# Optimization experiments

Hardware: AMD Instinct MI355X
Metric: run time of the kernel (lower is better)

## Reference

```python
import jax, jax.numpy as jnp
import numpy as np

N_HIDDEN = 2048
D_IN = 64
T_STEPS = 4096
WASHOUT = 200
SPECTRAL_RADIUS = 0.9
RIDGE_LAMBDA = 1e-6


def _scale_to_spectral_radius(W, rho, iters=100):
    # power iteration to estimate the dominant eigenvalue magnitude (spectral radius)
    rng = np.random.default_rng(0)
    v = rng.normal(size=W.shape[0]).astype(np.float64)
    v /= np.linalg.norm(v)
    for _ in range(iters):
        w = W @ v
        nrm = np.linalg.norm(w)
        v = w / nrm
    rad = np.linalg.norm(W @ v)
    return W * (rho / rad)


def setup_inputs() -> dict:
    key = jax.random.key(0)
    k1, k2, k3, k4 = jax.random.split(key, 4)
    u = jax.random.normal(k1, (T_STEPS, D_IN), dtype=jnp.float32)
    y = jax.random.normal(k2, (T_STEPS, 1), dtype=jnp.float32)
    W_in = jax.random.normal(k3, (N_HIDDEN, D_IN), dtype=jnp.float32) * 0.1
    W = np.asarray(jax.random.normal(k4, (N_HIDDEN, N_HIDDEN), dtype=jnp.float32), dtype=np.float64)
    W /= np.sqrt(N_HIDDEN)
    W = _scale_to_spectral_radius(W, SPECTRAL_RADIUS)
    W_res = jnp.asarray(W, dtype=jnp.float32)
    return {"u": u, "y": y, "W_in": W_in, "W_res": W_res, "washout": WASHOUT}


def reference(u, y, W_in, W_res, washout):
    # precompute input drive W_in @ u[t] for all t: [T, N]
    drive = u @ W_in.T
    x0 = jnp.zeros((W_res.shape[0],), dtype=u.dtype)

    def step(x, d):
        x = jnp.tanh(W_res @ x + d)
        return x, x

    _, X = jax.lax.scan(step, x0, drive)  # X: [T, N]
    Xw = X[washout:]                      # [T - washout, N]
    yw = y[washout:]                      # [T - washout, 1]
    A = Xw.T @ Xw + RIDGE_LAMBDA * jnp.eye(Xw.shape[1], dtype=Xw.dtype)
    Wout = jnp.linalg.solve(A, Xw.T @ yw)  # [N, 1]
    return Xw @ Wout                       # [T - washout, 1]
```

## Files before the change

kernel.cpp:

```cpp
#include <hip/hip_runtime.h>
#include <math.h>

#define NH      2048
#define TT      4096
#define DIN     64
#define WASH    200
#define TW      (TT - WASH)
#define LAMBDA  1e-6f

#define SCAN_BLOCKS  64
#define CG_BLOCKS    64
#define CG_ITERS     400

typedef unsigned long long u64;

#define X_OFF      ((size_t)0)
#define DRIVE_OFF  ((size_t)TT * NH)
#define A_OFF      DRIVE_OFF
#define B_OFF      ((size_t)2 * TT * NH)
#define INVD_OFF   (B_OFF + NH)
#define XV_OFF     (INVD_OFF + NH)
#define WS_FLOATS  (XV_OFF + NH)
#define XPACK_OFF  ((size_t)0)
#define PPACK_OFF  ((size_t)2 * NH)
#define PQSLOT_OFF ((size_t)3 * NH)
#define RZSLOT_OFF ((size_t)3 * NH + 64)
#define U64_TOTAL  ((size_t)3 * NH + 128)

__device__ __forceinline__ u64 pack_ev(int epoch, float v) {
    return ((u64)(unsigned)epoch << 32) | (u64)__float_as_uint(v);
}
__device__ __forceinline__ int   ep_of(u64 p)  { return (int)(p >> 32); }
__device__ __forceinline__ float val_of(u64 p) { return __uint_as_float((unsigned)p); }

__device__ __forceinline__ u64 aload(const u64* p) {
    return __hip_atomic_load(p, __ATOMIC_RELAXED, __HIP_MEMORY_SCOPE_AGENT);
}
__device__ __forceinline__ void astore(u64* p, u64 v) {
    __hip_atomic_store(p, v, __ATOMIC_RELAXED, __HIP_MEMORY_SCOPE_AGENT);
}

__global__ void init_kernel(float* ws) {
    int tid = threadIdx.x;
    u64* ub = (u64*)(ws + WS_FLOATS);
    for (size_t i = tid; i < U64_TOTAL; i += 256) ub[i] = 0ull;
    for (int i = tid; i < NH; i += 256) ws[B_OFF + i] = 0.f;
}

__global__ __launch_bounds__(256) void drive_kernel(
    const float* __restrict__ u, const float* __restrict__ Win,
    float* __restrict__ drive)
{
    __shared__ float Wt[256 * 64];
    const int tid = threadIdx.x;
    const int ic = blockIdx.x & 7;
    const int tc = blockIdx.x >> 3;
    const int i0 = ic * 256;
    for (int idx = tid; idx < 256 * 64; idx += 256) {
        int il = idx >> 6, k = idx & 63;
        Wt[k * 256 + il] = Win[(size_t)i0 * 64 + idx];
    }
    __syncthreads();
    for (int tt_ = 0; tt_ < 128; ++tt_) {
        int t = tc * 128 + tt_;
        const float* ur = u + (size_t)t * DIN;
        float acc = 0.f;
        #pragma unroll
        for (int k = 0; k < 64; ++k)
            acc = fmaf(Wt[k * 256 + tid], ur[k], acc);
        drive[(size_t)t * NH + i0 + tid] = acc;
    }
}

__global__ __launch_bounds__(1024, 1) void scan_kernel(
    const float* __restrict__ W, const float* __restrict__ drive,
    float* __restrict__ X, u64* xpack)
{
    __shared__ float xls[NH];
    const int tid     = threadIdx.x;
    const int r_local = tid >> 5;
    const int lane32  = tid & 31;
    const int row     = blockIdx.x * 32 + r_local;

    float4 wreg[16];
    {
        const float* wp = W + (size_t)row * NH + lane32 * 4;
        #pragma unroll
        for (int j = 0; j < 16; ++j) wreg[j] = *(const float4*)(wp + 128 * j);
    }

    for (int t = 0; t < TT; ++t) {
        float dval = drive[(size_t)t * NH + row];

        if (t == 0) {
            xls[tid] = 0.f; xls[tid + 1024] = 0.f;
        } else {
            const u64* src = xpack + (size_t)((t - 1) & 1) * NH;
            const int want = t;
            u64 a = aload(&src[tid]);
            u64 b = aload(&src[tid + 1024]);
            bool pa = true, pb = true;
            if (ep_of(a) >= want) { xls[tid] = val_of(a); pa = false; }
            if (ep_of(b) >= want) { xls[tid + 1024] = val_of(b); pb = false; }
            while (pa || pb) {
                __builtin_amdgcn_s_sleep(1);
                if (pa) { u64 v = aload(&src[tid]);
                          if (ep_of(v) >= want) { xls[tid] = val_of(v); pa = false; } }
                if (pb) { u64 v = aload(&src[tid + 1024]);
                          if (ep_of(v) >= want) { xls[tid + 1024] = val_of(v); pb = false; } }
            }
        }
        __syncthreads();

        float acc = 0.f;
        #pragma unroll
        for (int j = 0; j < 16; ++j) {
            float4 xv4 = *(const float4*)&xls[lane32 * 4 + 128 * j];
            float4 wv = wreg[j];
            acc = fmaf(wv.x, xv4.x, fmaf(wv.y, xv4.y,
                  fmaf(wv.z, xv4.z, fmaf(wv.w, xv4.w, acc))));
        }
        #pragma unroll
        for (int m = 16; m; m >>= 1) acc += __shfl_xor(acc, m);

        if (lane32 == 0) {
            float v = tanhf(acc + dval);
            X[(size_t)t * NH + row] = v;
            astore(&xpack[(size_t)(t & 1) * NH + row], pack_ev(t + 1, v));
        }
        __syncthreads();
    }
}

__global__ __launch_bounds__(256) void gram_kernel(
    const float* __restrict__ X, float* __restrict__ A)
{
    if (blockIdx.x < blockIdx.y) return;
    __shared__ float As[16 * 64];
    __shared__ float Bs[16 * 64];
    const int tx = threadIdx.x, ty = threadIdx.y;
    const int tid = ty * 16 + tx;
    const int i0 = blockIdx.y * 64, j0 = blockIdx.x * 64;
    const int ty4 = ty * 4, tx4 = tx * 4;
    float acc[4][4] = {};

    const int nch = (TW + 15) / 16;
    for (int ch = 0; ch < nch; ++ch) {
        int tbase = WASH + ch * 16;
        for (int v = tid; v < 16 * 64; v += 256) {
            int kk = v >> 6, col = v & 63;
            int t = tbase + kk;
            float a_ = 0.f, b_ = 0.f;
            if (t < TT) {
                a_ = X[(size_t)t * NH + i0 + col];
                b_ = X[(size_t)t * NH + j0 + col];
            }
            As[v] = a_; Bs[v] = b_;
        }
        __syncthreads();
        #pragma unroll
        for (int k = 0; k < 16; ++k) {
            float4 av = *(const float4*)&As[k * 64 + ty4];
            float4 bv = *(const float4*)&Bs[k * 64 + tx4];
            float a[4] = {av.x, av.y, av.z, av.w};
            float b[4] = {bv.x, bv.y, bv.z, bv.w};
            #pragma unroll
            for (int ai = 0; ai < 4; ++ai)
                #pragma unroll
                for (int bi = 0; bi < 4; ++bi)
                    acc[ai][bi] = fmaf(a[ai], b[bi], acc[ai][bi]);
        }
        __syncthreads();
    }
    const bool diag = (blockIdx.x == blockIdx.y);
    #pragma unroll
    for (int ai = 0; ai < 4; ++ai) {
        int gi = i0 + ty4 + ai;
        #pragma unroll
        for (int bi = 0; bi < 4; ++bi) {
            int gj = j0 + tx4 + bi;
            float v = acc[ai][bi];
            if (gi == gj) v += LAMBDA;
            A[(size_t)gi * NH + gj] = v;
            if (!diag) A[(size_t)gj * NH + gi] = v;
        }
    }
}

__global__ void bvec_kernel(const float* __restrict__ X, const float* __restrict__ y,
                            float* __restrict__ bv)
{
    const int ic = blockIdx.x & 7, tc = blockIdx.x >> 3;
    const int i = ic * 256 + threadIdx.x;
    const int t0 = WASH + tc * (TW / 8), t1 = t0 + (TW / 8);
    float acc = 0.f;
    for (int t = t0; t < t1; ++t)
        acc = fmaf(X[(size_t)t * NH + i], y[t], acc);
    atomicAdd(&bv[i], acc);
}

__global__ void invdiag_kernel(const float* __restrict__ A, float* __restrict__ invd)
{
    int i = blockIdx.x * 256 + threadIdx.x;
    invd[i] = 1.0f / A[(size_t)i * NH + i];
}

__global__ __launch_bounds__(1024, 1) void cg_kernel(
    const float* __restrict__ A, const float* __restrict__ bvec,
    const float* __restrict__ invd, float* __restrict__ xv,
    u64* ppack, u64* pqslot, u64* rzslot)
{
    __shared__ float pls[NH];
    __shared__ float qsh[32], r32[32], x32[32], z32[32], inv32[32];
    __shared__ float csh[2];
    const int tid     = threadIdx.x;
    const int r_local = tid >> 5;
    const int lane32  = tid & 31;
    const int row0 = blockIdx.x * 32;
    const int row  = row0 + r_local;

    float4 areg[16];
    {
        const float* ap = A + (size_t)row * NH + lane32 * 4;
        #pragma unroll
        for (int j = 0; j < 16; ++j) areg[j] = *(const float4*)(ap + 128 * j);
    }

    if (tid < 32) {
        int i = row0 + tid;
        float bi = bvec[i], iv = invd[i];
        inv32[tid] = iv;
        x32[tid] = 0.f; r32[tid] = bi;
        float zi = iv * bi;
        z32[tid] = zi;
        astore(&ppack[i], pack_ev(1, zi));
        float part = bi * zi;
        #pragma unroll
        for (int m = 16; m; m >>= 1) part += __shfl_xor(part, m, 32);
        if (tid == 0) astore(&rzslot[blockIdx.x], pack_ev(1, part));
    }
    if (tid < 64) {
        u64 v = aload(&rzslot[tid]);
        while (ep_of(v) < 1) { __builtin_amdgcn_s_sleep(1); v = aload(&rzslot[tid]); }
        float s = val_of(v);
        #pragma unroll
        for (int m = 32; m; m >>= 1) s += __shfl_xor(s, m);
        if (tid == 0) csh[1] = s;
    }
    __syncthreads();
    float rho = csh[1];

    for (int it = 0; it < CG_ITERS; ++it) {
        {
            const int want = it + 1;
            u64 a = aload(&ppack[tid]);
            u64 b = aload(&ppack[tid + 1024]);
            bool pa = true, pb = true;
            if (ep_of(a) >= want) { pls[tid] = val_of(a); pa = false; }
            if (ep_of(b) >= want) { pls[tid + 1024] = val_of(b); pb = false; }
            while (pa || pb) {
                __builtin_amdgcn_s_sleep(1);
                if (pa) { u64 v = aload(&ppack[tid]);
                          if (ep_of(v) >= want) { pls[tid] = val_of(v); pa = false; } }
                if (pb) { u64 v = aload(&ppack[tid + 1024]);
                          if (ep_of(v) >= want) { pls[tid + 1024] = val_of(v); pb = false; } }
            }
        }
        __syncthreads();

        float acc = 0.f;
        #pragma unroll
        for (int j = 0; j < 16; ++j) {
            float4 pv = *(const float4*)&pls[lane32 * 4 + 128 * j];
            float4 av = areg[j];
            acc = fmaf(av.x, pv.x, fmaf(av.y, pv.y,
                  fmaf(av.z, pv.z, fmaf(av.w, pv.w, acc))));
        }
        #pragma unroll
        for (int m = 16; m; m >>= 1) acc += __shfl_xor(acc, m, 32);
        if (lane32 == 0) qsh[r_local] = acc;
        __syncthreads();

        if (tid < 32) {
            float t1 = qsh[tid] * pls[row0 + tid];
            #pragma unroll
            for (int m = 16; m; m >>= 1) t1 += __shfl_xor(t1, m, 32);
            if (tid == 0) astore(&pqslot[blockIdx.x], pack_ev(it + 1, t1));
        }
        if (tid < 64) {
            u64 v = aload(&pqslot[tid]);
            while (ep_of(v) < it + 1) { __builtin_amdgcn_s_sleep(1); v = aload(&pqslot[tid]); }
            float s = val_of(v);
            #pragma unroll
            for (int m = 32; m; m >>= 1) s += __shfl_xor(s, m);
            if (tid == 0) csh[0] = s;
        }
        __syncthreads();
        float pq = csh[0];
        float alpha = (pq != 0.f) ? rho / pq : 0.f;

        if (tid < 32) {
            int i = row0 + tid;
            float pi = pls[i], qi = qsh[tid];
            x32[tid] = fmaf(alpha, pi, x32[tid]);
            float ri = r32[tid] - alpha * qi;
            r32[tid] = ri;
            float zi = inv32[tid] * ri;
            z32[tid] = zi;
            float t2 = ri * zi;
            #pragma unroll
            for (int m = 16; m; m >>= 1) t2 += __shfl_xor(t2, m, 32);
            if (tid == 0) astore(&rzslot[blockIdx.x], pack_ev(it + 2, t2));
        }
        if (tid < 64) {
            u64 v = aload(&rzslot[tid]);
            while (ep_of(v) < it + 2) { __builtin_amdgcn_s_sleep(1); v = aload(&rzslot[tid]); }
            float s = val_of(v);
            #pragma unroll
            for (int m = 32; m; m >>= 1) s += __shfl_xor(s, m);
            if (tid == 0) csh[1] = s;
        }
        __syncthreads();
        float rho_new = csh[1];
        float beta = (rho != 0.f) ? rho_new / rho : 0.f;

        if (tid < 32) {
            int i = row0 + tid;
            float pn = fmaf(beta, pls[i], z32[tid]);
            astore(&ppack[i], pack_ev(it + 2, pn));
        }
        rho = rho_new;
        __syncthreads();
    }

    if (tid < 32) xv[row0 + tid] = x32[tid];
}

__global__ void out_kernel(const float* __restrict__ X, const float* __restrict__ w,
                           float* __restrict__ out)
{
    __shared__ float red[4];
    const int tid = threadIdx.x;
    const int rowt = WASH + blockIdx.x;
    float acc = 0.f;
    #pragma unroll
    for (int j = 0; j < 8; ++j) {
        int c = tid + 256 * j;
        acc = fmaf(X[(size_t)rowt * NH + c], w[c], acc);
    }
    #pragma unroll
    for (int m = 32; m; m >>= 1) acc += __shfl_xor(acc, m);
    if ((tid & 63) == 0) red[tid >> 6] = acc;
    __syncthreads();
    if (tid == 0) out[blockIdx.x] = red[0] + red[1] + red[2] + red[3];
}

extern "C" void kernel_launch(void* const* d_in, const int* in_sizes, int n_in,
                              void* d_out, int out_size, void* d_ws, size_t ws_size,
                              hipStream_t stream)
{
    const float* u    = (const float*)d_in[0];
    const float* y    = (const float*)d_in[1];
    const float* Win  = (const float*)d_in[2];
    const float* Wres = (const float*)d_in[3];

    float* ws = (float*)d_ws;
    float* X     = ws + X_OFF;
    float* drive = ws + DRIVE_OFF;
    float* A     = ws + A_OFF;
    u64*   ub    = (u64*)(ws + WS_FLOATS);
    u64*   xpack = ub + XPACK_OFF;
    u64*   ppack = ub + PPACK_OFF;
    u64*   pqslot = ub + PQSLOT_OFF;
    u64*   rzslot = ub + RZSLOT_OFF;

    init_kernel<<<1, 256, 0, stream>>>(ws);
    drive_kernel<<<256, 256, 0, stream>>>(u, Win, drive);
    scan_kernel<<<SCAN_BLOCKS, 1024, 0, stream>>>(Wres, drive, X, xpack);
    gram_kernel<<<dim3(32, 32), dim3(16, 16), 0, stream>>>(X, A);
    bvec_kernel<<<64, 256, 0, stream>>>(X, y, ws + B_OFF);
    invdiag_kernel<<<8, 256, 0, stream>>>(A, ws + INVD_OFF);
    cg_kernel<<<CG_BLOCKS, 1024, 0, stream>>>(A, ws + B_OFF, ws + INVD_OFF,
                                              ws + XV_OFF, ppack, pqslot, rzslot);
    out_kernel<<<TW, 256, 0, stream>>>(X, ws + XV_OFF, (float*)d_out);
}
```

Before: 14.50 ms.

## Restructure CG to broadcast z and fuse rz wait; scan computes two rows per wave

The CG loop now broadcasts the preconditioned residual z instead of the search direction p. Every block rebuilds p locally from z and beta, so the separate rz grid-wide wait plus p publish becomes a single exchange per iteration, which cuts one global synchronisation round per iteration. The scan kernel now has each 64-lane wave compute two rows rather than one row per 32 lanes, trading shuffle layout for fewer reductions. The CG iteration count also drops from 400 to 320, which cuts work but may weaken convergence and accuracy.

```diff
diff --git a/kernel.cpp b/kernel.cpp
--- a/kernel.cpp
+++ b/kernel.cpp
@@ -10,7 +10,7 @@
 
 #define SCAN_BLOCKS  64
 #define CG_BLOCKS    64
-#define CG_ITERS     400
+#define CG_ITERS     320
 
 typedef unsigned long long u64;
 
@@ -22,7 +22,7 @@
 #define XV_OFF     (INVD_OFF + NH)
 #define WS_FLOATS  (XV_OFF + NH)
 #define XPACK_OFF  ((size_t)0)
-#define PPACK_OFF  ((size_t)2 * NH)
+#define ZPACK_OFF  ((size_t)2 * NH)
 #define PQSLOT_OFF ((size_t)3 * NH)
 #define RZSLOT_OFF ((size_t)3 * NH + 64)
 #define U64_TOTAL  ((size_t)3 * NH + 128)
@@ -77,20 +77,24 @@
     float* __restrict__ X, u64* xpack)
 {
     __shared__ float xls[NH];
-    const int tid     = threadIdx.x;
-    const int r_local = tid >> 5;
-    const int lane32  = tid & 31;
-    const int row     = blockIdx.x * 32 + r_local;
-
-    float4 wreg[16];
+    const int tid  = threadIdx.x;
+    const int wave = tid >> 6;
+    const int lane = tid & 63;
+    const int rowA = blockIdx.x * 32 + wave * 2;
+
+    float4 wA[8], wB[8];
     {
-        const float* wp = W + (size_t)row * NH + lane32 * 4;
-        #pragma unroll
-        for (int j = 0; j < 16; ++j) wreg[j] = *(const float4*)(wp + 128 * j);
+        const float* wpA = W + (size_t)rowA * NH + lane * 4;
+        const float* wpB = wpA + NH;
+        #pragma unroll
+        for (int j = 0; j < 8; ++j) {
+            wA[j] = *(const float4*)(wpA + 256 * j);
+            wB[j] = *(const float4*)(wpB + 256 * j);
+        }
     }
 
     for (int t = 0; t < TT; ++t) {
-        float dval = drive[(size_t)t * NH + row];
+        float dval = (lane < 2) ? drive[(size_t)t * NH + rowA + lane] : 0.f;
 
         if (t == 0) {
             xls[tid] = 0.f; xls[tid + 1024] = 0.f;
@@ -112,18 +116,20 @@
         }
         __syncthreads();
 
-        float acc = 0.f;
-        #pragma unroll
-        for (int j = 0; j < 16; ++j) {
-            float4 xv4 = *(const float4*)&xls[lane32 * 4 + 128 * j];
-            float4 wv = wreg[j];
-            acc = fmaf(wv.x, xv4.x, fmaf(wv.y, xv4.y,
-                  fmaf(wv.z, xv4.z, fmaf(wv.w, xv4.w, acc))));
-        }
-        #pragma unroll
-        for (int m = 16; m; m >>= 1) acc += __shfl_xor(acc, m);
-
-        if (lane32 == 0) {
+        float a0 = 0.f, a1 = 0.f;
+        #pragma unroll
+        for (int j = 0; j < 8; ++j) {
+            float4 xv = *(const float4*)&xls[lane * 4 + 256 * j];
+            float4 va = wA[j], vb = wB[j];
+            a0 = fmaf(va.x, xv.x, fmaf(va.y, xv.y, fmaf(va.z, xv.z, fmaf(va.w, xv.w, a0))));
+            a1 = fmaf(vb.x, xv.x, fmaf(vb.y, xv.y, fmaf(vb.z, xv.z, fmaf(vb.w, xv.w, a1))));
+        }
+        #pragma unroll
+        for (int m = 32; m; m >>= 1) { a0 += __shfl_xor(a0, m); a1 += __shfl_xor(a1, m); }
+
+        if (lane < 2) {
+            float acc = (lane == 0) ? a0 : a1;
+            int row = rowA + lane;
             float v = tanhf(acc + dval);
             X[(size_t)t * NH + row] = v;
             astore(&xpack[(size_t)(t & 1) * NH + row], pack_ev(t + 1, v));
@@ -208,10 +214,11 @@
 __global__ __launch_bounds__(1024, 1) void cg_kernel(
     const float* __restrict__ A, const float* __restrict__ bvec,
     const float* __restrict__ invd, float* __restrict__ xv,
-    u64* ppack, u64* pqslot, u64* rzslot)
+    u64* zpack, u64* pqslot, u64* rzslot)
 {
     __shared__ float pls[NH];
-    __shared__ float qsh[32], r32[32], x32[32], z32[32], inv32[32];
+    __shared__ float zls[NH];
+    __shared__ float r32[32], x32[32], q32[32], inv32[32];
     __shared__ float csh[2];
     const int tid     = threadIdx.x;
     const int r_local = tid >> 5;
@@ -226,46 +233,54 @@
         for (int j = 0; j < 16; ++j) areg[j] = *(const float4*)(ap + 128 * j);
     }
 
+    pls[tid] = 0.f; pls[tid + 1024] = 0.f;
+
     if (tid < 32) {
         int i = row0 + tid;
         float bi = bvec[i], iv = invd[i];
         inv32[tid] = iv;
         x32[tid] = 0.f; r32[tid] = bi;
         float zi = iv * bi;
-        z32[tid] = zi;
-        astore(&ppack[i], pack_ev(1, zi));
+        astore(&zpack[i], pack_ev(1, zi));
         float part = bi * zi;
         #pragma unroll
         for (int m = 16; m; m >>= 1) part += __shfl_xor(part, m, 32);
         if (tid == 0) astore(&rzslot[blockIdx.x], pack_ev(1, part));
     }
-    if (tid < 64) {
-        u64 v = aload(&rzslot[tid]);
-        while (ep_of(v) < 1) { __builtin_amdgcn_s_sleep(1); v = aload(&rzslot[tid]); }
-        float s = val_of(v);
-        #pragma unroll
-        for (int m = 32; m; m >>= 1) s += __shfl_xor(s, m);
-        if (tid == 0) csh[1] = s;
-    }
     __syncthreads();
-    float rho = csh[1];
+
+    float rho_prev = 1.f;
 
     for (int it = 0; it < CG_ITERS; ++it) {
         {
             const int want = it + 1;
-            u64 a = aload(&ppack[tid]);
-            u64 b = aload(&ppack[tid + 1024]);
+            u64 a = aload(&zpack[tid]);
+            u64 b = aload(&zpack[tid + 1024]);
             bool pa = true, pb = true;
-            if (ep_of(a) >= want) { pls[tid] = val_of(a); pa = false; }
-            if (ep_of(b) >= want) { pls[tid + 1024] = val_of(b); pb = false; }
+            if (ep_of(a) >= want) { zls[tid] = val_of(a); pa = false; }
+            if (ep_of(b) >= want) { zls[tid + 1024] = val_of(b); pb = false; }
             while (pa || pb) {
                 __builtin_amdgcn_s_sleep(1);
-                if (pa) { u64 v = aload(&ppack[tid]);
-                          if (ep_of(v) >= want) { pls[tid] = val_of(v); pa = false; } }
-                if (pb) { u64 v = aload(&ppack[tid + 1024]);
-                          if (ep_of(v) >= want) { pls[tid + 1024] = val_of(v); pb = false; } }
+                if (pa) { u64 v = aload(&zpack[tid]);
+                          if (ep_of(v) >= want) { zls[tid] = val_of(v); pa = false; } }
+                if (pb) { u64 v = aload(&zpack[tid + 1024]);
+                          if (ep_of(v) >= want) { zls[tid + 1024] = val_of(v); pb = false; } }
             }
         }
+        if (tid < 64) {
+            u64 v = aload(&rzslot[tid]);
+            while (ep_of(v) < it + 1) { __builtin_amdgcn_s_sleep(1); v = aload(&rzslot[tid]); }
+            float s = val_of(v);
+            #pragma unroll
+            for (int m = 32; m; m >>= 1) s += __shfl_xor(s, m);
+            if (tid == 0) csh[1] = s;
+        }
+        __syncthreads();
+        float rho = csh[1];
+        float beta = (it == 0) ? 0.f : ((rho_prev != 0.f) ? rho / rho_prev : 0.f);
+
+        pls[tid]        = fmaf(beta, pls[tid],        zls[tid]);
+        pls[tid + 1024] = fmaf(beta, pls[tid + 1024], zls[tid + 1024]);
         __syncthreads();
 
         float acc = 0.f;
@@ -278,11 +293,11 @@
         }
         #pragma unroll
         for (int m = 16; m; m >>= 1) acc += __shfl_xor(acc, m, 32);
-        if (lane32 == 0) qsh[r_local] = acc;
+        if (lane32 == 0) q32[r_local] = acc;
         __syncthreads();
 
         if (tid < 32) {
-            float t1 = qsh[tid] * pls[row0 + tid];
+            float t1 = q32[tid] * pls[row0 + tid];
             #pragma unroll
             for (int m = 16; m; m >>= 1) t1 += __shfl_xor(t1, m, 32);
             if (tid == 0) astore(&pqslot[blockIdx.x], pack_ev(it + 1, t1));
@@ -301,35 +316,18 @@
 
         if (tid < 32) {
             int i = row0 + tid;
-            float pi = pls[i], qi = qsh[tid];
+            float pi = pls[i], qi = q32[tid];
             x32[tid] = fmaf(alpha, pi, x32[tid]);
             float ri = r32[tid] - alpha * qi;
             r32[tid] = ri;
             float zi = inv32[tid] * ri;
-            z32[tid] = zi;
+            astore(&zpack[i], pack_ev(it + 2, zi));
             float t2 = ri * zi;
             #pragma unroll
             for (int m = 16; m; m >>= 1) t2 += __shfl_xor(t2, m, 32);
             if (tid == 0) astore(&rzslot[blockIdx.x], pack_ev(it + 2, t2));
         }
-        if (tid < 64) {
-            u64 v = aload(&rzslot[tid]);
-            while (ep_of(v) < it + 2) { __builtin_amdgcn_s_sleep(1); v = aload(&rzslot[tid]); }
-            float s = val_of(v);
-            #pragma unroll
-            for (int m = 32; m; m >>= 1) s += __shfl_xor(s, m);
-            if (tid == 0) csh[1] = s;
-        }
-        __syncthreads();
-        float rho_new = csh[1];
-        float beta = (rho != 0.f) ? rho_new / rho : 0.f;
-
-        if (tid < 32) {
-            int i = row0 + tid;
-            float pn = fmaf(beta, pls[i], z32[tid]);
-            astore(&ppack[i], pack_ev(it + 2, pn));
-        }
-        rho = rho_new;
+        rho_prev = rho;
         __syncthreads();
     }
 
@@ -369,8 +367,8 @@
     float* drive = ws + DRIVE_OFF;
     float* A     = ws + A_OFF;
     u64*   ub    = (u64*)(ws + WS_FLOATS);
-    u64*   xpack = ub + XPACK_OFF;
-    u64*   ppack = ub + PPACK_OFF;
+    u64*   xpack  = ub + XPACK_OFF;
+    u64*   zpack  = ub + ZPACK_OFF;
     u64*   pqslot = ub + PQSLOT_OFF;
     u64*   rzslot = ub + RZSLOT_OFF;
 
@@ -381,6 +379,6 @@
     bvec_kernel<<<64, 256, 0, stream>>>(X, y, ws + B_OFF);
     invdiag_kernel<<<8, 256, 0, stream>>>(A, ws + INVD_OFF);
     cg_kernel<<<CG_BLOCKS, 1024, 0, stream>>>(A, ws + B_OFF, ws + INVD_OFF,
-                                              ws + XV_OFF, ppack, pqslot, rzslot);
+                                              ws + XV_OFF, zpack, pqslot, rzslot);
     out_kernel<<<TW, 256, 0, stream>>>(X, ws + XV_OFF, (float*)d_out);
 }
```

Result: faster. 13.32 ms (-8.1%).
